# Kernel tuning notes

Measured on AMD Instinct MI355X. Metric: run time of the kernel, lower is better.

The kernel has to match this reference:

```python
import jax, jax.numpy as jnp
import numpy as np

EMBED_DIM = 256
NUM_HEADS = 4
HEAD_DIM = EMBED_DIM // NUM_HEADS  # 64
FEAT_X = FEAT_Y = 64               # 64*64 = 4096 tokens
THETA = 10000.0


def _axial_cos_sin(dim, end_x, end_y, theta):
    # compute_axial_cis: dim//4 frequencies per spatial axis, concatenated -> [N, dim//2]
    f = 1.0 / (theta ** (np.arange(0, dim, 4)[: dim // 4].astype(np.float32) / dim))
    t = np.arange(end_x * end_y)
    tx = (t % end_x).astype(np.float32)
    ty = (t // end_x).astype(np.float32)
    ang = np.concatenate([np.outer(tx, f), np.outer(ty, f)], axis=-1)  # [N, dim//2]
    return jnp.asarray(np.cos(ang)), jnp.asarray(np.sin(ang))


def _apply_rope(x, cos, sin):
    # x: [B, H, N, D]; adjacent pairs (x[..., 2i], x[..., 2i+1]) are the complex parts
    xr = x.reshape(*x.shape[:-1], -1, 2)
    xa, xb = xr[..., 0], xr[..., 1]          # [B, H, N, D//2]
    oa = xa * cos - xb * sin                  # cos/sin: [N, D//2], broadcast
    ob = xa * sin + xb * cos
    return jnp.stack([oa, ob], axis=-1).reshape(x.shape)


def setup_inputs() -> dict:
    key = jax.random.key(0)
    ks = jax.random.split(key, 8)
    B, N, D = 1, FEAT_X * FEAT_Y, EMBED_DIM
    s = 0.02  # weight init scale
    return {
        "q": jax.random.normal(ks[0], (B, N, D), jnp.float32),
        "k": jax.random.normal(ks[1], (B, N, D), jnp.float32),
        "v": jax.random.normal(ks[2], (B, N, D), jnp.float32),
        "wq": jax.random.normal(ks[3], (D, D), jnp.float32) * s,
        "bq": jnp.zeros((D,), jnp.float32),
        "wk": jax.random.normal(ks[4], (D, D), jnp.float32) * s,
        "bk": jnp.zeros((D,), jnp.float32),
        "wv": jax.random.normal(ks[5], (D, D), jnp.float32) * s,
        "bv": jnp.zeros((D,), jnp.float32),
        "wo": jax.random.normal(ks[6], (D, D), jnp.float32) * s,
        "bo": jnp.zeros((D,), jnp.float32),
        "return_attn": 0,
        "num_k_exclude_rope": 0,
    }


def reference(q, k, v, wq, bq, wk, bk, wv, bv, wo, bo, return_attn, num_k_exclude_rope):
    B, Nq, D = q.shape
    H, hd = NUM_HEADS, HEAD_DIM
    # QKV projections (weights stored [in, out], equiv to torch Linear W.T)
    qp = (q @ wq + bq).reshape(B, Nq, H, hd).transpose(0, 2, 1, 3)   # [B,H,Nq,hd]
    kp = (k @ wk + bk).reshape(B, -1, H, hd).transpose(0, 2, 1, 3)   # [B,H,Nk,hd]
    vp = (v @ wv + bv).reshape(B, -1, H, hd).transpose(0, 2, 1, 3)
    # rotary encoding on q and the first (Nk - num_k_exclude_rope) keys
    cos, sin = _axial_cos_sin(hd, FEAT_X, FEAT_Y, THETA)
    qp = _apply_rope(qp, cos, sin)
    nkr = kp.shape[2] - num_k_exclude_rope  # static Python int
    if num_k_exclude_rope > 0:
        kp = jnp.concatenate([_apply_rope(kp[:, :, :nkr], cos, sin), kp[:, :, nkr:]], axis=2)
    else:
        kp = _apply_rope(kp, cos, sin)
    # SDPA (eval: dropout_p = 0)
    scale = 1.0 / jnp.sqrt(jnp.asarray(hd, qp.dtype))
    scores = jnp.einsum("bhqd,bhkd->bhqk", qp, kp) * scale
    attn = jax.nn.softmax(scores, axis=-1)
    out = jnp.einsum("bhqk,bhkd->bhqd", attn, vp)
    out = out.transpose(0, 2, 1, 3).reshape(B, Nq, D)
    out = out @ wo + bo
    if return_attn:
        return out, scores  # attn_weight = q @ k^T * scale (pre-softmax, as in source)
    return out
```

## Files before the change

### kernel.cpp

```cpp
#include <hip/hip_runtime.h>
#include <hip/hip_bf16.h>
#include <math.h>

#define NTOK 4096
#define DEMB 256
#define NHEAD 4
#define HD 64

typedef short bf16x8 __attribute__((ext_vector_type(8)));
typedef short bf16x4 __attribute__((ext_vector_type(4)));
typedef float f32x4 __attribute__((ext_vector_type(4)));

__device__ __forceinline__ unsigned short f2b(float f) {
  union { float f; unsigned u; } v; v.f = f;
  return (unsigned short)((v.u + 0x7FFFu + ((v.u >> 16) & 1u)) >> 16);
}
__device__ __forceinline__ unsigned cvtpk(float lo, float hi) {
  unsigned r;
  asm("v_cvt_pk_bf16_f32 %0, %1, %2" : "=v"(r) : "v"(lo), "v"(hi));
  return r;
}

__global__ __launch_bounds__(256) void prep_kernel(
    const float* wq, const float* wk, const float* wv, const float* wo,
    unsigned short* wt, float2* cs) {
  int b = blockIdx.x;
  if (b < 64) {
    int m = b >> 4, tile = b & 15;
    int ti = tile >> 2, tj = tile & 3;
    const float* w = (m == 0) ? wq : (m == 1) ? wk : (m == 2) ? wv : wo;
    __shared__ float tl[64][65];
    int r = threadIdx.x >> 2, c4 = threadIdx.x & 3;
#pragma unroll
    for (int j = 0; j < 4; ++j) {
      float4 v4 = *(const float4*)(w + (ti * 64 + r) * 256 + tj * 64 + c4 * 16 + j * 4);
      tl[r][c4 * 16 + j * 4 + 0] = v4.x;
      tl[r][c4 * 16 + j * 4 + 1] = v4.y;
      tl[r][c4 * 16 + j * 4 + 2] = v4.z;
      tl[r][c4 * 16 + j * 4 + 3] = v4.w;
    }
    __syncthreads();
    unsigned short* dst = wt + m * 65536 + (tj * 64 + r) * 256 + ti * 64 + c4 * 16;
    bf16x8 o0, o1;
#pragma unroll
    for (int j = 0; j < 8; ++j) o0[j] = (short)f2b(tl[c4 * 16 + j][r]);
#pragma unroll
    for (int j = 0; j < 8; ++j) o1[j] = (short)f2b(tl[c4 * 16 + 8 + j][r]);
    *(bf16x8*)dst = o0;
    *(bf16x8*)(dst + 8) = o1;
  } else {
    int idx = (b - 64) * 256 + threadIdx.x;
    int n = idx >> 5, p = idx & 31;
    int j = p & 15;
    float f = powf(10000.0f, -(float)j / 16.0f);
    float ang = ((p < 16) ? (float)(n & 63) : (float)(n >> 6)) * f;
    cs[idx] = make_float2(cosf(ang), sinf(ang));
  }
}

__global__ __launch_bounds__(256) void qkvproj_kernel(
    const float* q, const float* k, const float* v, const unsigned short* wt,
    const float* bq, const float* bk, const float* bv, const float2* cs,
    unsigned short* qp, unsigned short* kp, unsigned short* vt) {
  int which = blockIdx.z;
  int wave = threadIdx.x >> 6, lane = threadIdx.x & 63;
  int col = lane & 15, g = lane >> 4;
  int mbase = blockIdx.x * 64 + wave * 16;
  int nbase = blockIdx.y * 64;
  const float* X = (which == 0) ? q : (which == 1) ? k : v;
  const unsigned short* W = wt + which * 65536;
  const float* bias = (which == 0) ? bq : (which == 1) ? bk : bv;

  f32x4 acc[4] = {};
  const float* ap0 = X + (mbase + col) * 256 + g * 8;
#pragma unroll
  for (int ks = 0; ks < 256; ks += 32) {
    float4 a0 = *(const float4*)(ap0 + ks);
    float4 a1 = *(const float4*)(ap0 + ks + 4);
    bf16x8 af;
    af[0] = (short)f2b(a0.x); af[1] = (short)f2b(a0.y);
    af[2] = (short)f2b(a0.z); af[3] = (short)f2b(a0.w);
    af[4] = (short)f2b(a1.x); af[5] = (short)f2b(a1.y);
    af[6] = (short)f2b(a1.z); af[7] = (short)f2b(a1.w);
#pragma unroll
    for (int nt = 0; nt < 4; ++nt) {
      bf16x8 bf_ = *(const bf16x8*)(W + (nbase + nt * 16 + col) * 256 + ks + g * 8);
      acc[nt] = __builtin_amdgcn_mfma_f32_16x16x32_bf16(af, bf_, acc[nt], 0, 0, 0);
    }
  }

  if (which == 2) {
    int kpos = ((mbase >> 5) << 5) + 8 * g + 4 * ((mbase >> 4) & 1);
#pragma unroll
    for (int nt = 0; nt < 4; ++nt) {
      int c = nbase + nt * 16 + col;
      float b = bias[c];
      bf16x4 pk;
#pragma unroll
      for (int r = 0; r < 4; ++r) pk[r] = (short)f2b(acc[nt][r] + b);
      *(bf16x4*)(vt + c * NTOK + kpos) = pk;
    }
  } else {
    const float QSC = 0.18033688f;
    unsigned short* dst = (which == 0) ? qp : kp;
#pragma unroll
    for (int nt = 0; nt < 4; ++nt) {
      int c = nbase + nt * 16 + col;
      float b = bias[c];
#pragma unroll
      for (int r = 0; r < 4; ++r) {
        int t = mbase + g * 4 + r;
        float val = acc[nt][r] + b;
        float2 csv = cs[t * 32 + ((c & 63) >> 1)];
        float pv = __shfl_xor(val, 1);
        float sn = (c & 1) ? csv.y : -csv.y;
        val = val * csv.x + pv * sn;
        if (which == 0) val *= QSC;
        dst[((c >> 6) * NTOK + t) * HD + (c & 63)] = f2b(val);
      }
    }
  }
}

__global__ __launch_bounds__(512, 4) void attn_kernel(
    const unsigned short* qp, const unsigned short* kp,
    const unsigned short* vt, float* pO, float* pml) {
  __shared__ alignas(16) unsigned char lds[32768];
  int id = blockIdx.x;
  int xcd = id & 7;
  int head = xcd >> 1;
  int rest = id >> 3;
  int qtile = rest >> 2;
  int ks = (xcd & 1) * 4 + (rest & 3);
  int qb = qtile * 256;
  int slot = (head * 16 + qtile) * 8 + ks;
  int w = threadIdx.x >> 6, lane = threadIdx.x & 63;
  int col = lane & 15, g = lane >> 4;
  int stok = threadIdx.x >> 3, spart = threadIdx.x & 7;
  unsigned soff = (unsigned)(stok * 128) +
                  (unsigned)((spart * 16) ^ ((stok & 7) << 4));

  const unsigned short* kgp = kp + (head * NTOK + ks * 512) * HD;
  const unsigned short* vgp = vt + head * HD * NTOK + ks * 512;

  bf16x8 skr, svr;
  auto stage_issue = [&](int t) {
    skr = *(const bf16x8*)(kgp + (t * 64 + stok) * HD + spart * 8);
    svr = *(const bf16x8*)(vgp + stok * NTOK + t * 64 + spart * 8);
  };
  auto stage_write = [&](int buf) {
    *(bf16x8*)(lds + (unsigned)buf * 16384u + soff) = skr;
    *(bf16x8*)(lds + (unsigned)buf * 16384u + 8192u + soff) = svr;
  };

  bf16x8 ones;
#pragma unroll
  for (int i = 0; i < 8; ++i) ones[i] = (short)0x3F80;

  bf16x8 qf[2][2];
  {
    const unsigned short* qr = qp + (head * NTOK + qb + w * 32) * HD;
#pragma unroll
    for (int qt = 0; qt < 2; ++qt)
#pragma unroll
      for (int h2 = 0; h2 < 2; ++h2)
        qf[qt][h2] = *(const bf16x8*)(qr + (qt * 16 + col) * HD + h2 * 32 + g * 8);
  }

  stage_issue(0);
  stage_write(0);
  stage_issue(1);
  __syncthreads();

  f32x4 acco[4][2] = {};
  f32x4 lacc[2] = {};

  for (int t = 0; t < 8; ++t) {
    int cur = t & 1;
    unsigned kb = (unsigned)cur * 16384u, vb = (unsigned)cur * 16384u + 8192u;

    f32x4 st[4][2] = {};
#pragma unroll
    for (int mt = 0; mt < 4; ++mt) {
      int tok = mt * 16 + col;
      unsigned ro = kb + (unsigned)(tok * 128) + (unsigned)((g * 16) ^ ((tok & 7) << 4));
      bf16x8 kf0 = *(const bf16x8*)(lds + ro);
      bf16x8 kf1 = *(const bf16x8*)(lds + (ro ^ 64u));
#pragma unroll
      for (int qt = 0; qt < 2; ++qt) {
        st[mt][qt] = __builtin_amdgcn_mfma_f32_16x16x32_bf16(kf0, qf[qt][0], st[mt][qt], 0, 0, 0);
        st[mt][qt] = __builtin_amdgcn_mfma_f32_16x16x32_bf16(kf1, qf[qt][1], st[mt][qt], 0, 0, 0);
      }
    }

    if (t < 7) {
      stage_write(cur ^ 1);
      if (t < 6) stage_issue(t + 2);
    }

    unsigned pw[2][2][4];
#pragma unroll
    for (int qt = 0; qt < 2; ++qt) {
      float p[4][4];
#pragma unroll
      for (int mt = 0; mt < 4; ++mt)
#pragma unroll
        for (int r = 0; r < 4; ++r) p[mt][r] = exp2f(st[mt][qt][r]);
#pragma unroll
      for (int kk = 0; kk < 2; ++kk) {
        pw[qt][kk][0] = cvtpk(p[2 * kk][0], p[2 * kk][1]);
        pw[qt][kk][1] = cvtpk(p[2 * kk][2], p[2 * kk][3]);
        pw[qt][kk][2] = cvtpk(p[2 * kk + 1][0], p[2 * kk + 1][1]);
        pw[qt][kk][3] = cvtpk(p[2 * kk + 1][2], p[2 * kk + 1][3]);
      }
    }

#pragma unroll
    for (int kk = 0; kk < 2; ++kk) {
      union { unsigned u[4]; bf16x8 v; } pf[2];
#pragma unroll
      for (int qt = 0; qt < 2; ++qt) {
        pf[qt].u[0] = pw[qt][kk][0]; pf[qt].u[1] = pw[qt][kk][1];
        pf[qt].u[2] = pw[qt][kk][2]; pf[qt].u[3] = pw[qt][kk][3];
        lacc[qt] = __builtin_amdgcn_mfma_f32_16x16x32_bf16(pf[qt].v, ones, lacc[qt], 0, 0, 0);
      }
#pragma unroll
      for (int nt = 0; nt < 4; ++nt) {
        int d = nt * 16 + col;
        unsigned off = vb + (unsigned)(d * 128) +
                       (unsigned)((kk * 64 + g * 16) ^ ((d & 7) << 4));
        bf16x8 vf = *(const bf16x8*)(lds + off);
#pragma unroll
        for (int qt = 0; qt < 2; ++qt)
          acco[nt][qt] = __builtin_amdgcn_mfma_f32_16x16x32_bf16(pf[qt].v, vf, acco[nt][qt], 0, 0, 0);
      }
    }
    __syncthreads();
  }

#pragma unroll
  for (int nt = 0; nt < 4; ++nt)
#pragma unroll
    for (int qt = 0; qt < 2; ++qt)
#pragma unroll
      for (int r = 0; r < 4; ++r)
        pO[slot * 16384 + (w * 32 + qt * 16 + g * 4 + r) * 64 + nt * 16 + col] =
            acco[nt][qt][r];
  if (col == 0) {
#pragma unroll
    for (int qt = 0; qt < 2; ++qt)
#pragma unroll
      for (int r = 0; r < 4; ++r)
        pml[slot * 256 + w * 32 + qt * 16 + g * 4 + r] = lacc[qt][r];
  }
}

__global__ __launch_bounds__(256) void merge_kernel(
    const float* pO, const float* pml, unsigned short* att) {
  int bid = blockIdx.x;
  int group = bid >> 2, quarter = bid & 3;
  int head = group >> 4, qtile = group & 15;
  int t = threadIdx.x;
  int qloc = quarter * 64 + (t >> 2);
  int d0 = (t & 3) * 16;
  float den = 0.f, num[16] = {};
#pragma unroll
  for (int ks = 0; ks < 8; ++ks) {
    den += pml[(group * 8 + ks) * 256 + qloc];
    const float* ob = pO + (group * 8 + ks) * 16384 + qloc * 64 + d0;
#pragma unroll
    for (int i = 0; i < 16; ++i) num[i] += ob[i];
  }
  float inv = 1.0f / den;
  union { unsigned short s[16]; bf16x8 v[2]; } ov;
#pragma unroll
  for (int i = 0; i < 16; ++i) ov.s[i] = f2b(num[i] * inv);
  unsigned short* dst = att + (qtile * 256 + qloc) * DEMB + head * HD + d0;
  *(bf16x8*)dst = ov.v[0];
  *(bf16x8*)(dst + 8) = ov.v[1];
}

__global__ __launch_bounds__(256) void outproj_kernel(
    const unsigned short* att, const unsigned short* wt_o, const float* bo,
    float* out) {
  int wave = threadIdx.x >> 6, lane = threadIdx.x & 63;
  int col = lane & 15, g = lane >> 4;
  int mbase = blockIdx.x * 64 + wave * 16;
  int nbase = blockIdx.y * 64;
  f32x4 acc[4] = {};
#pragma unroll
  for (int ks = 0; ks < 256; ks += 32) {
    bf16x8 af = *(const bf16x8*)(att + (mbase + col) * 256 + ks + g * 8);
#pragma unroll
    for (int nt = 0; nt < 4; ++nt) {
      bf16x8 bf_ = *(const bf16x8*)(wt_o + (nbase + nt * 16 + col) * 256 + ks + g * 8);
      acc[nt] = __builtin_amdgcn_mfma_f32_16x16x32_bf16(af, bf_, acc[nt], 0, 0, 0);
    }
  }
#pragma unroll
  for (int nt = 0; nt < 4; ++nt) {
    int c = nbase + nt * 16 + col;
    float b = bo[c];
#pragma unroll
    for (int r = 0; r < 4; ++r)
      out[(mbase + g * 4 + r) * 256 + c] = acc[nt][r] + b;
  }
}

extern "C" void kernel_launch(void* const* d_in, const int* in_sizes, int n_in,
                              void* d_out, int out_size, void* d_ws, size_t ws_size,
                              hipStream_t stream) {
  const float* q  = (const float*)d_in[0];
  const float* k  = (const float*)d_in[1];
  const float* v  = (const float*)d_in[2];
  const float* wq = (const float*)d_in[3];
  const float* bq = (const float*)d_in[4];
  const float* wk = (const float*)d_in[5];
  const float* bk = (const float*)d_in[6];
  const float* wv = (const float*)d_in[7];
  const float* bv = (const float*)d_in[8];
  const float* wo = (const float*)d_in[9];
  const float* bo = (const float*)d_in[10];
  float* out = (float*)d_out;

  char* ws = (char*)d_ws;
  float2* cs         = (float2*)ws;
  unsigned short* wt = (unsigned short*)(ws + (1u << 20));
  unsigned short* qp = (unsigned short*)(ws + 1536u * 1024u);
  unsigned short* kp = qp + NHEAD * NTOK * HD;
  unsigned short* vt = kp + NHEAD * NTOK * HD;
  unsigned short* att = vt + NHEAD * NTOK * HD;
  float* pO  = (float*)(ws + 9728u * 1024u);
  float* pml = (float*)(ws + 43008u * 1024u);

  prep_kernel<<<576, 256, 0, stream>>>(wq, wk, wv, wo, wt, cs);
  qkvproj_kernel<<<dim3(64, 4, 3), 256, 0, stream>>>(q, k, v, wt, bq, bk, bv, cs,
                                                     qp, kp, vt);
  attn_kernel<<<512, 512, 0, stream>>>(qp, kp, vt, pO, pml);
  merge_kernel<<<256, 256, 0, stream>>>(pO, pml, att);
  outproj_kernel<<<dim3(64, 4), 256, 0, stream>>>(att, wt + 3 * 65536, bo, out);
}
```

Baseline: 74.80 us.

## Fuse split-K merge into output projection, store partials as bf16, halve attention blocks

The separate merge kernel is removed. The output projection now reduces the eight split-K partial outputs and denominators into a swizzled LDS tile before its MFMA loop. Partial outputs are stored in bf16 with a token-major layout so each row's partials sit next to each other, which cuts the write and read traffic. The attention kernel moves to 256-thread blocks covering 128 query rows, with twice as many blocks. Each thread now stages two chunks of K and V. The trade-off is extra rounding of the partial sums to bf16, and a merge that is repeated for each of the two column blocks of the output projection.

```diff
diff --git a/kernel.cpp b/kernel.cpp
--- a/kernel.cpp
+++ b/kernel.cpp
@@ -122,35 +122,41 @@
   }
 }
 
-__global__ __launch_bounds__(512, 4) void attn_kernel(
+__global__ __launch_bounds__(256, 4) void attn_kernel(
     const unsigned short* qp, const unsigned short* kp,
-    const unsigned short* vt, float* pO, float* pml) {
+    const unsigned short* vt, unsigned short* pO, float* pml) {
   __shared__ alignas(16) unsigned char lds[32768];
   int id = blockIdx.x;
   int xcd = id & 7;
   int head = xcd >> 1;
   int rest = id >> 3;
-  int qtile = rest >> 2;
+  int qt128 = rest >> 2;
   int ks = (xcd & 1) * 4 + (rest & 3);
-  int qb = qtile * 256;
-  int slot = (head * 16 + qtile) * 8 + ks;
+  int qb = qt128 * 128;
   int w = threadIdx.x >> 6, lane = threadIdx.x & 63;
   int col = lane & 15, g = lane >> 4;
-  int stok = threadIdx.x >> 3, spart = threadIdx.x & 7;
-  unsigned soff = (unsigned)(stok * 128) +
-                  (unsigned)((spart * 16) ^ ((stok & 7) << 4));
 
   const unsigned short* kgp = kp + (head * NTOK + ks * 512) * HD;
   const unsigned short* vgp = vt + head * HD * NTOK + ks * 512;
 
-  bf16x8 skr, svr;
+  bf16x8 skr[2], svr[2];
   auto stage_issue = [&](int t) {
-    skr = *(const bf16x8*)(kgp + (t * 64 + stok) * HD + spart * 8);
-    svr = *(const bf16x8*)(vgp + stok * NTOK + t * 64 + spart * 8);
+#pragma unroll
+    for (int i = 0; i < 2; ++i) {
+      int c = (int)threadIdx.x + i * 256, tok = c >> 3, part = c & 7;
+      skr[i] = *(const bf16x8*)(kgp + (t * 64 + tok) * HD + part * 8);
+      svr[i] = *(const bf16x8*)(vgp + tok * NTOK + t * 64 + part * 8);
+    }
   };
   auto stage_write = [&](int buf) {
-    *(bf16x8*)(lds + (unsigned)buf * 16384u + soff) = skr;
-    *(bf16x8*)(lds + (unsigned)buf * 16384u + 8192u + soff) = svr;
+#pragma unroll
+    for (int i = 0; i < 2; ++i) {
+      int c = (int)threadIdx.x + i * 256, tok = c >> 3, part = c & 7;
+      unsigned soff = (unsigned)(tok * 128) +
+                      (unsigned)((part * 16) ^ ((tok & 7) << 4));
+      *(bf16x8*)(lds + (unsigned)buf * 16384u + soff) = skr[i];
+      *(bf16x8*)(lds + (unsigned)buf * 16384u + 8192u + soff) = svr[i];
+    }
   };
 
   bf16x8 ones;
@@ -243,67 +249,81 @@
 #pragma unroll
     for (int qt = 0; qt < 2; ++qt)
 #pragma unroll
-      for (int r = 0; r < 4; ++r)
-        pO[slot * 16384 + (w * 32 + qt * 16 + g * 4 + r) * 64 + nt * 16 + col] =
-            acco[nt][qt][r];
+      for (int r = 0; r < 4; ++r) {
+        int row = qb + w * 32 + qt * 16 + g * 4 + r;
+        pO[((head * NTOK + row) * 8 + ks) * 64 + nt * 16 + col] =
+            f2b(acco[nt][qt][r]);
+      }
   if (col == 0) {
 #pragma unroll
     for (int qt = 0; qt < 2; ++qt)
 #pragma unroll
-      for (int r = 0; r < 4; ++r)
-        pml[slot * 256 + w * 32 + qt * 16 + g * 4 + r] = lacc[qt][r];
-  }
-}
-
-__global__ __launch_bounds__(256) void merge_kernel(
-    const float* pO, const float* pml, unsigned short* att) {
-  int bid = blockIdx.x;
-  int group = bid >> 2, quarter = bid & 3;
-  int head = group >> 4, qtile = group & 15;
+      for (int r = 0; r < 4; ++r) {
+        int row = qb + w * 32 + qt * 16 + g * 4 + r;
+        pml[(head * NTOK + row) * 8 + ks] = lacc[qt][r];
+      }
+  }
+}
+
+__global__ __launch_bounds__(256) void outproj_kernel(
+    const unsigned short* pO, const float* pml, const unsigned short* wt_o,
+    const float* bo, float* out) {
+  __shared__ alignas(16) unsigned char attl[8192];
+  int mbase = blockIdx.x * 16;
+  int nbase = blockIdx.y * 128;
   int t = threadIdx.x;
-  int qloc = quarter * 64 + (t >> 2);
-  int d0 = (t & 3) * 16;
-  float den = 0.f, num[16] = {};
-#pragma unroll
-  for (int ks = 0; ks < 8; ++ks) {
-    den += pml[(group * 8 + ks) * 256 + qloc];
-    const float* ob = pO + (group * 8 + ks) * 16384 + qloc * 64 + d0;
-#pragma unroll
-    for (int i = 0; i < 16; ++i) num[i] += ob[i];
-  }
-  float inv = 1.0f / den;
-  union { unsigned short s[16]; bf16x8 v[2]; } ov;
-#pragma unroll
-  for (int i = 0; i < 16; ++i) ov.s[i] = f2b(num[i] * inv);
-  unsigned short* dst = att + (qtile * 256 + qloc) * DEMB + head * HD + d0;
-  *(bf16x8*)dst = ov.v[0];
-  *(bf16x8*)(dst + 8) = ov.v[1];
-}
-
-__global__ __launch_bounds__(256) void outproj_kernel(
-    const unsigned short* att, const unsigned short* wt_o, const float* bo,
-    float* out) {
-  int wave = threadIdx.x >> 6, lane = threadIdx.x & 63;
+  {
+    int r = t >> 4, rest = t & 15;
+    int h = rest >> 2, dq = rest & 3;
+    int row = mbase + r;
+    const float* mlp = pml + (h * NTOK + row) * 8;
+    float den = 0.f;
+#pragma unroll
+    for (int ks = 0; ks < 8; ++ks) den += mlp[ks];
+    float num[16] = {};
+    const unsigned short* ob = pO + (h * NTOK + row) * 8 * 64 + dq * 16;
+#pragma unroll
+    for (int ks = 0; ks < 8; ++ks) {
+      union { bf16x8 v; unsigned short s[8]; } a0, a1;
+      a0.v = *(const bf16x8*)(ob + ks * 64);
+      a1.v = *(const bf16x8*)(ob + ks * 64 + 8);
+#pragma unroll
+      for (int i = 0; i < 8; ++i) {
+        num[i]     += __uint_as_float((unsigned)a0.s[i] << 16);
+        num[8 + i] += __uint_as_float((unsigned)a1.s[i] << 16);
+      }
+    }
+    float inv = 1.0f / den;
+    union { unsigned short s[16]; bf16x8 v[2]; } ov;
+#pragma unroll
+    for (int i = 0; i < 16; ++i) ov.s[i] = f2b(num[i] * inv);
+    unsigned base = (unsigned)(r * 512 + h * 128 + dq * 32);
+    unsigned x = (unsigned)((r & 7) << 4);
+    *(bf16x8*)(attl + (base ^ x)) = ov.v[0];
+    *(bf16x8*)(attl + ((base + 16u) ^ x)) = ov.v[1];
+  }
+  __syncthreads();
+  int w = t >> 6, lane = t & 63;
   int col = lane & 15, g = lane >> 4;
-  int mbase = blockIdx.x * 64 + wave * 16;
-  int nbase = blockIdx.y * 64;
-  f32x4 acc[4] = {};
+  f32x4 acc[2] = {};
 #pragma unroll
   for (int ks = 0; ks < 256; ks += 32) {
-    bf16x8 af = *(const bf16x8*)(att + (mbase + col) * 256 + ks + g * 8);
-#pragma unroll
-    for (int nt = 0; nt < 4; ++nt) {
-      bf16x8 bf_ = *(const bf16x8*)(wt_o + (nbase + nt * 16 + col) * 256 + ks + g * 8);
-      acc[nt] = __builtin_amdgcn_mfma_f32_16x16x32_bf16(af, bf_, acc[nt], 0, 0, 0);
-    }
-  }
-#pragma unroll
-  for (int nt = 0; nt < 4; ++nt) {
-    int c = nbase + nt * 16 + col;
+    unsigned ab = (unsigned)(col * 512 + ks * 2 + g * 16) ^
+                  (unsigned)((col & 7) << 4);
+    bf16x8 af = *(const bf16x8*)(attl + ab);
+#pragma unroll
+    for (int ct = 0; ct < 2; ++ct) {
+      bf16x8 bf_ = *(const bf16x8*)(wt_o + (nbase + w * 32 + ct * 16 + col) * 256 + ks + g * 8);
+      acc[ct] = __builtin_amdgcn_mfma_f32_16x16x32_bf16(af, bf_, acc[ct], 0, 0, 0);
+    }
+  }
+#pragma unroll
+  for (int ct = 0; ct < 2; ++ct) {
+    int c = nbase + w * 32 + ct * 16 + col;
     float b = bo[c];
 #pragma unroll
     for (int r = 0; r < 4; ++r)
-      out[(mbase + g * 4 + r) * 256 + c] = acc[nt][r] + b;
+      out[(mbase + g * 4 + r) * 256 + c] = acc[ct][r] + b;
   }
 }
 
@@ -329,14 +349,12 @@
   unsigned short* qp = (unsigned short*)(ws + 1536u * 1024u);
   unsigned short* kp = qp + NHEAD * NTOK * HD;
   unsigned short* vt = kp + NHEAD * NTOK * HD;
-  unsigned short* att = vt + NHEAD * NTOK * HD;
-  float* pO  = (float*)(ws + 9728u * 1024u);
-  float* pml = (float*)(ws + 43008u * 1024u);
+  unsigned short* pO = (unsigned short*)(ws + 9728u * 1024u);
+  float* pml = (float*)(ws + 26624u * 1024u);
 
   prep_kernel<<<576, 256, 0, stream>>>(wq, wk, wv, wo, wt, cs);
   qkvproj_kernel<<<dim3(64, 4, 3), 256, 0, stream>>>(q, k, v, wt, bq, bk, bv, cs,
                                                      qp, kp, vt);
-  attn_kernel<<<512, 512, 0, stream>>>(qp, kp, vt, pO, pml);
-  merge_kernel<<<256, 256, 0, stream>>>(pO, pml, att);
-  outproj_kernel<<<dim3(64, 4), 256, 0, stream>>>(att, wt + 3 * 65536, bo, out);
-}
+  attn_kernel<<<1024, 256, 0, stream>>>(qp, kp, vt, pO, pml);
+  outproj_kernel<<<dim3(256, 2), 256, 0, stream>>>(pO, pml, wt + 3 * 65536, bo, out);
+}
```

Measured after the change: 68.75 us, median of 3. -8.1%, faster.
